# Optimization experiments

Hardware: AMD Instinct MI355X
Metric: run time of the kernel (lower is better)

Reference implementation:

```python
import jax, jax.numpy as jnp
import numpy as np

N = 100000
NFEAT = 128
NHID = 128
NCLASS = 40
E = 1600000
EPS = 1e-5


def _spmm(vals, src, dst, x, n):
    # y[dst] += vals * x[src]  (sparse adj @ x)
    return jax.ops.segment_sum(vals[:, None] * x[src], dst, num_segments=n)


def _bn(h, gamma, beta, rmean, rvar):
    # BatchNorm1d in eval mode (running statistics)
    return (h - rmean) * jax.lax.rsqrt(rvar + EPS) * gamma + beta


def setup_inputs() -> dict:
    key = jax.random.key(0)
    ks = jax.random.split(key, 24)
    inp = {
        'x': jax.random.normal(ks[0], (N, NFEAT), dtype=jnp.float32),
        'M': jax.random.uniform(ks[1], (N, 1), dtype=jnp.float32),
        'AM': jax.random.uniform(ks[2], (N, 1), dtype=jnp.float32),
        'srcZ': jax.random.randint(ks[3], (E,), 0, N, dtype=jnp.int32),
        'dstZ': jax.random.randint(ks[4], (E,), 0, N, dtype=jnp.int32),
        'valsZ': jax.random.uniform(ks[5], (E,), dtype=jnp.float32),
        'src': jax.random.randint(ks[6], (E,), 0, N, dtype=jnp.int32),
        'dst': jax.random.randint(ks[7], (E,), 0, N, dtype=jnp.int32),
        'vals': jax.random.uniform(ks[8], (E,), dtype=jnp.float32),
        # layer 0 (PaGConv) params
        'W0': jax.random.normal(ks[9], (NHID, NFEAT), dtype=jnp.float32) * (1.414 / np.sqrt(NFEAT)),
        'b0': jnp.zeros((NHID,), dtype=jnp.float32),
        'g0': jnp.ones((NHID,), dtype=jnp.float32),
        'be0': jnp.zeros((NHID,), dtype=jnp.float32),
        'rm0': jax.random.normal(ks[10], (NHID,), dtype=jnp.float32) * 0.1,
        'rv0': jax.random.uniform(ks[11], (NHID,), dtype=jnp.float32) + 0.5,
        # layer 1 (GConv) params
        'W1': jax.random.normal(ks[12], (NHID, NHID), dtype=jnp.float32) * (1.414 / np.sqrt(NHID)),
        'b1': jnp.zeros((NHID,), dtype=jnp.float32),
        'g1': jnp.ones((NHID,), dtype=jnp.float32),
        'be1': jnp.zeros((NHID,), dtype=jnp.float32),
        'rm1': jax.random.normal(ks[13], (NHID,), dtype=jnp.float32) * 0.1,
        'rv1': jax.random.uniform(ks[14], (NHID,), dtype=jnp.float32) + 0.5,
        # layer 2 (GConv) params
        'W2': jax.random.normal(ks[15], (NCLASS, NHID), dtype=jnp.float32) * (1.414 / np.sqrt(NHID)),
        'b2': jnp.zeros((NCLASS,), dtype=jnp.float32),
    }
    return inp


def reference(x, M, AM, srcZ, dstZ, valsZ, src, dst, vals,
              W0, b0, g0, be0, rm0, rv0,
              W1, b1, g1, be1, rm1, rv1,
              W2, b2):
    n = x.shape[0]
    # layer 0: PaGConv with adjZ: fc(spmm(adjZ, M*x) * AM), then BN + ReLU (dropout off in eval)
    h = _spmm(valsZ, srcZ, dstZ, M * x, n) * AM
    h = h @ W0.T + b0
    h = jax.nn.relu(_bn(h, g0, be0, rm0, rv0))
    # layer 1: GConv with adj: fc(spmm(adj, h)), then BN + ReLU
    h = _spmm(vals, src, dst, h, n)
    h = h @ W1.T + b1
    h = jax.nn.relu(_bn(h, g1, be1, rm1, rv1))
    # layer 2: GConv, then log_softmax
    h = _spmm(vals, src, dst, h, n)
    h = h @ W2.T + b2
    return jax.nn.log_softmax(h, axis=-1)
```

## Files before the change

kernel.cpp:

```cpp
#include <hip/hip_runtime.h>
#include <math.h>

#define NFEAT 128
#define NCLS 40
#define NCLSP 64
#define BINROWS 64
#define NBINMAX 1600
#define NBLKC 256
#define CHUNKMAX 6400
#define SEGC 7
#define RSMAX 2048

typedef short bf16x8 __attribute__((ext_vector_type(8)));
typedef float f32x4 __attribute__((ext_vector_type(4)));

__device__ __forceinline__ float bf2f(unsigned int lo16) {
  return __uint_as_float((lo16 & 0xffffu) << 16);
}
__device__ __forceinline__ unsigned int f2bf(float x) {
  unsigned int u = __float_as_uint(x);
  return (u + 0x7fffu + ((u >> 16) & 1u)) >> 16;
}

__global__ __launch_bounds__(256) void prep_all(
    const float* b0, const float* g0, const float* be0,
    const float* rm0, const float* rv0,
    const float* b1, const float* g1, const float* be1,
    const float* rm1, const float* rv1,
    float* sc0, float* sh0, float* sc1, float* sh1,
    const float* __restrict__ W0, const float* __restrict__ W1,
    const float* __restrict__ W2,
    unsigned short* __restrict__ Wb0, unsigned short* __restrict__ Wb1,
    unsigned short* __restrict__ W2hi, unsigned short* __restrict__ W2lo,
    const float* __restrict__ x, const float* __restrict__ Mv,
    unsigned short* __restrict__ xm, int n) {
  int t = threadIdx.x;
  if (blockIdx.x == 0) {
    if (t < 128) {
      float s = g0[t] * rsqrtf(rv0[t] + 1e-5f);
      sc0[t] = s;
      sh0[t] = (b0[t] - rm0[t]) * s + be0[t];
    } else {
      int i = t - 128;
      float s = g1[i] * rsqrtf(rv1[i] + 1e-5f);
      sc1[i] = s;
      sh1[i] = (b1[i] - rm1[i]) * s + be1[i];
    }
    return;
  }
  if (blockIdx.x <= 20) {
    int i = (blockIdx.x - 1) * 256 + t;
    if (i < 4096) {
      const float* W = (i < 2048) ? W0 : W1;
      unsigned short* Wb = (i < 2048) ? Wb0 : Wb1;
      int j = (i < 2048) ? i : i - 2048;
      const float4* p = (const float4*)(W + (size_t)j * 8);
      float4 v0 = p[0], v1 = p[1];
      unsigned int o0 = f2bf(v0.x) | (f2bf(v0.y) << 16);
      unsigned int o1 = f2bf(v0.z) | (f2bf(v0.w) << 16);
      unsigned int o2 = f2bf(v1.x) | (f2bf(v1.y) << 16);
      unsigned int o3 = f2bf(v1.z) | (f2bf(v1.w) << 16);
      ((uint4*)Wb)[j] = make_uint4(o0, o1, o2, o3);
    } else {
      int j = i - 4096;
      int r = j >> 4;
      float v[8] = {0.f, 0.f, 0.f, 0.f, 0.f, 0.f, 0.f, 0.f};
      if (r < NCLS) {
        const float4* p = (const float4*)(W2 + (size_t)j * 8);
        float4 a = p[0], b = p[1];
        v[0] = a.x; v[1] = a.y; v[2] = a.z; v[3] = a.w;
        v[4] = b.x; v[5] = b.y; v[6] = b.z; v[7] = b.w;
      }
      unsigned int h[8], l[8];
#pragma unroll
      for (int q = 0; q < 8; ++q) {
        h[q] = f2bf(v[q]);
        l[q] = f2bf(v[q] - bf2f(h[q]));
      }
      ((uint4*)W2hi)[j] = make_uint4(h[0] | (h[1] << 16), h[2] | (h[3] << 16),
                                     h[4] | (h[5] << 16), h[6] | (h[7] << 16));
      ((uint4*)W2lo)[j] = make_uint4(l[0] | (l[1] << 16), l[2] | (l[3] << 16),
                                     l[4] | (l[5] << 16), l[6] | (l[7] << 16));
    }
    return;
  }
  int i = (blockIdx.x - 21) * 256 + t;
  if (i >= n * (NFEAT / 8)) return;
  int row = i >> 4;
  float m = Mv[row];
  const float4* p = (const float4*)(x + (size_t)i * 8);
  float4 v0 = p[0], v1 = p[1];
  unsigned int o0 = f2bf(v0.x * m) | (f2bf(v0.y * m) << 16);
  unsigned int o1 = f2bf(v0.z * m) | (f2bf(v0.w * m) << 16);
  unsigned int o2 = f2bf(v1.x * m) | (f2bf(v1.y * m) << 16);
  unsigned int o3 = f2bf(v1.z * m) | (f2bf(v1.w * m) << 16);
  ((uint4*)xm)[i] = make_uint4(o0, o1, o2, o3);
}

__global__ __launch_bounds__(256) void bin_sort2(
    const int* __restrict__ srcZ, const int* __restrict__ dstZ, const float* __restrict__ valZ,
    const int* __restrict__ srcA, const int* __restrict__ dstA, const float* __restrict__ valA,
    int2* __restrict__ DrmZ, int2* __restrict__ DrmA,
    int2* __restrict__ binsCZ, int2* __restrict__ binsCA,
    int E, int nbin, int chunk) {
  __shared__ int2 stage[CHUNKMAX];
  __shared__ int cur[NBINMAX];
  __shared__ int ps[256];
  const int t = threadIdx.x;
  int k = blockIdx.x;
  const int* srcp; const int* dstp; const float* valp; int2* Drm; int2* binsC;
  if (k < NBLKC) {
    srcp = srcZ; dstp = dstZ; valp = valZ; Drm = DrmZ; binsC = binsCZ;
  } else {
    k -= NBLKC;
    srcp = srcA; dstp = dstA; valp = valA; Drm = DrmA; binsC = binsCA;
  }
  for (int i = t; i < nbin; i += 256) cur[i] = 0;
  __syncthreads();
  const int e0 = k * chunk, e1 = min(E, e0 + chunk);
#pragma unroll 4
  for (int e = e0 + t; e < e1; e += 256) atomicAdd(&cur[dstp[e] >> 6], 1);
  __syncthreads();
  int loc[SEGC], cnt[SEGC];
  int s = 0;
#pragma unroll
  for (int j = 0; j < SEGC; ++j) {
    int i = t * SEGC + j;
    int v = (i < nbin) ? cur[i] : 0;
    loc[j] = s; cnt[j] = v;
    s += v;
  }
  ps[t] = s;
  __syncthreads();
  for (int o = 1; o < 256; o <<= 1) {
    int x = (t >= o) ? ps[t - o] : 0;
    __syncthreads();
    ps[t] += x;
    __syncthreads();
  }
  int ex = ps[t] - s;
#pragma unroll
  for (int j = 0; j < SEGC; ++j) {
    int i = t * SEGC + j;
    if (i < nbin) {
      int o = ex + loc[j];
      Drm[(size_t)k * nbin + i] = make_int2(e0 + o, cnt[j]);
      cur[i] = o;
    }
  }
  __syncthreads();
#pragma unroll 2
  for (int e = e0 + t; e < e1; e += 256) {
    int d = dstp[e];
    int p = atomicAdd(&cur[d >> 6], 1);
    stage[p] = make_int2(srcp[e] | ((d & 63) << 17), __float_as_int(valp[e]));
  }
  __syncthreads();
  const int n = e1 - e0;
  for (int i = t; i < n; i += 256) binsC[e0 + i] = stage[i];
}

__global__ __launch_bounds__(256) void row_sort2(
    const int2* __restrict__ DrmZ, const int2* __restrict__ DrmA,
    const int2* __restrict__ binsCZ, const int2* __restrict__ binsCA,
    int2* __restrict__ bins2Z, int2* __restrict__ bins2A,
    int2* __restrict__ rdZ, int2* __restrict__ rdA, int n, int nbin) {
  __shared__ int2 stage[RSMAX];
  __shared__ int ps[256];
  __shared__ int rcnt[BINROWS];
  __shared__ int roff[BINROWS];
  int b = blockIdx.x;
  const int t = threadIdx.x;
  const int2* Drm; const int2* binsC; int2* bins2; int2* rowdesc;
  if (b < nbin) {
    Drm = DrmZ; binsC = binsCZ; bins2 = bins2Z; rowdesc = rdZ;
  } else {
    b -= nbin;
    Drm = DrmA; binsC = binsCA; bins2 = bins2A; rowdesc = rdA;
  }
  if (t < BINROWS) rcnt[t] = 0;
  int2 run = Drm[(size_t)t * nbin + b];
  ps[t] = run.y;
  __syncthreads();
  for (int o = 1; o < 256; o <<= 1) {
    int x = (t >= o) ? ps[t - o] : 0;
    __syncthreads();
    ps[t] += x;
    __syncthreads();
  }
  int mystart = ps[t] - run.y;
  for (int j = 0; j < run.y; ++j) {
    int2 en = binsC[run.x + j];
    int idx = mystart + j;
    if (idx < RSMAX) stage[idx] = en;
    atomicAdd(&rcnt[(en.x >> 17) & 63], 1);
  }
  __syncthreads();
  const int bs = b * RSMAX;
  if (t < BINROWS) {
    int c = rcnt[t];
    int s = c;
#pragma unroll
    for (int o = 1; o < 64; o <<= 1) {
      int v = __shfl_up(s, o);
      if (t >= o) s += v;
    }
    int excl = s - c;
    int row = b * BINROWS + t;
    if (row < n) rowdesc[row] = make_int2(bs + excl, c);
    roff[t] = excl;
  }
  __syncthreads();
  int total = min(ps[255], RSMAX);
  for (int i = t; i < total; i += 256) {
    int2 en = stage[i];
    int row = (en.x >> 17) & 63;
    int p = atomicAdd(&roff[row], 1);
    bins2[bs + p] = en;
  }
}

template <bool SCALE>
__global__ __launch_bounds__(256) void spmm128_sorted(
    const int2* __restrict__ rowdesc, const int2* __restrict__ bins2,
    const unsigned short* __restrict__ X, const float* __restrict__ AM,
    unsigned short* __restrict__ Y, int n) {
  int row = (blockIdx.x * 256 + threadIdx.x) >> 6;
  int lane = threadIdx.x & 63;
  if (row >= n) return;
  int2 rd = rowdesc[row];
  int s = rd.x, d = rd.y;
  int half = lane >> 5, l32 = lane & 31;
  float s0 = 0.f, s1 = 0.f, s2 = 0.f, s3 = 0.f;
  for (int kb = 0; kb < d; kb += 64) {
    int rem = min(64, d - kb);
    int2 my = (lane < rem) ? bins2[s + kb + lane] : make_int2(0, 0);
    int myc = my.x & 0x1FFFF;
    float myw = __int_as_float(my.y);
    for (int k = 0; k < rem; k += 8) {
#pragma unroll
      for (int st = 0; st < 4; ++st) {
        int idx = k + 2 * st + half;
        int c = __shfl(myc, idx);
        float wv = __shfl(myw, idx);
        uint2 pv = *(const uint2*)(X + (size_t)c * NFEAT + l32 * 4);
        s0 += wv * bf2f(pv.x);
        s1 += wv * bf2f(pv.x >> 16);
        s2 += wv * bf2f(pv.y);
        s3 += wv * bf2f(pv.y >> 16);
      }
    }
  }
  s0 += __shfl_xor(s0, 32); s1 += __shfl_xor(s1, 32);
  s2 += __shfl_xor(s2, 32); s3 += __shfl_xor(s3, 32);
  if (SCALE) {
    float am = AM[row];
    s0 *= am; s1 *= am; s2 *= am; s3 *= am;
  }
  unsigned int pk = half ? (f2bf(s2) | (f2bf(s3) << 16)) : (f2bf(s0) | (f2bf(s1) << 16));
  ((unsigned int*)Y)[(size_t)row * (NFEAT / 2) + l32 * 2 + half] = pk;
}

template <bool FUSE_G2>
__global__ __launch_bounds__(256) void gemm_mfma128(
    const unsigned short* __restrict__ Y, const unsigned short* __restrict__ Wb,
    const float* __restrict__ scale, const float* __restrict__ shift,
    unsigned short* __restrict__ Out,
    const unsigned short* __restrict__ Whi, const unsigned short* __restrict__ Wlo,
    unsigned short* __restrict__ G2, int M) {
  const int wave = threadIdx.x >> 6;
  const int lane = threadIdx.x & 63;
  const int quad = lane >> 4;
  const int l16 = lane & 15;
  const int arow = blockIdx.x * 64 + wave * 16 + l16;
  const bool rv = arow < M;

  f32x4 acc[8];
#pragma unroll
  for (int c = 0; c < 8; ++c) acc[c] = (f32x4){0.f, 0.f, 0.f, 0.f};

#pragma unroll
  for (int kc = 0; kc < 128; kc += 32) {
    bf16x8 a = rv ? *(const bf16x8*)(Y + (size_t)arow * 128 + kc + quad * 8)
                  : (bf16x8){0, 0, 0, 0, 0, 0, 0, 0};
#pragma unroll
    for (int c = 0; c < 8; ++c) {
      bf16x8 b = *(const bf16x8*)(Wb + (size_t)(c * 16 + l16) * 128 + kc + quad * 8);
      acc[c] = __builtin_amdgcn_mfma_f32_16x16x32_bf16(a, b, acc[c], 0, 0, 0);
    }
  }

  const int orow0 = blockIdx.x * 64 + wave * 16 + quad * 4;

  if constexpr (!FUSE_G2) {
#pragma unroll
    for (int c = 0; c < 8; ++c) {
      int col = c * 16 + l16;
      float sc = scale[col], sh = shift[col];
#pragma unroll
      for (int r = 0; r < 4; ++r) {
        int orow = orow0 + r;
        if (orow < M) {
          float v = fmaxf(acc[c][r] * sc + sh, 0.f);
          Out[(size_t)orow * 128 + col] = (unsigned short)f2bf(v);
        }
      }
    }
  } else {
    __shared__ unsigned short Ht[64][136];
    const int lrow0 = wave * 16 + quad * 4;
#pragma unroll
    for (int c = 0; c < 8; ++c) {
      int col = c * 16 + l16;
      float sc = scale[col], sh = shift[col];
#pragma unroll
      for (int r = 0; r < 4; ++r) {
        float v = fmaxf(acc[c][r] * sc + sh, 0.f);
        Ht[lrow0 + r][col] = (unsigned short)f2bf(v);
      }
    }
    __syncthreads();
    bf16x8 af[4];
#pragma unroll
    for (int kc = 0; kc < 4; ++kc)
      af[kc] = *(const bf16x8*)(&Ht[wave * 16 + l16][kc * 32 + quad * 8]);
    f32x4 acc2[4];
#pragma unroll
    for (int c2 = 0; c2 < 4; ++c2) acc2[c2] = (f32x4){0.f, 0.f, 0.f, 0.f};
#pragma unroll
    for (int kc = 0; kc < 4; ++kc) {
#pragma unroll
      for (int c2 = 0; c2 < 4; ++c2) {
        bf16x8 bh = *(const bf16x8*)(Whi + (size_t)(c2 * 16 + l16) * 128 + kc * 32 + quad * 8);
        bf16x8 bl = *(const bf16x8*)(Wlo + (size_t)(c2 * 16 + l16) * 128 + kc * 32 + quad * 8);
        acc2[c2] = __builtin_amdgcn_mfma_f32_16x16x32_bf16(af[kc], bh, acc2[c2], 0, 0, 0);
        acc2[c2] = __builtin_amdgcn_mfma_f32_16x16x32_bf16(af[kc], bl, acc2[c2], 0, 0, 0);
      }
    }
#pragma unroll
    for (int c2 = 0; c2 < 4; ++c2) {
      int col = c2 * 16 + l16;
#pragma unroll
      for (int r = 0; r < 4; ++r) {
        int orow = orow0 + r;
        if (orow < M) G2[(size_t)orow * NCLSP + col] = (unsigned short)f2bf(acc2[c2][r]);
      }
    }
  }
}

__global__ __launch_bounds__(256) void spmm_softmax64(
    const int2* __restrict__ rowdesc, const int2* __restrict__ bins2,
    const unsigned short* __restrict__ G2, const float* __restrict__ b2,
    float* __restrict__ out, int n) {
  int row = (blockIdx.x * 256 + threadIdx.x) >> 6;
  int lane = threadIdx.x & 63;
  if (row >= n) return;
  const int eidx = lane >> 4, q = lane & 15;
  const bool vq = q < (NCLS / 4);
  float4 bv = vq ? *(const float4*)(b2 + q * 4) : make_float4(0.f, 0.f, 0.f, 0.f);

  int2 rdv = rowdesc[row];
  int s0i = rdv.x, d = rdv.y;
  float a0 = 0.f, a1 = 0.f, a2 = 0.f, a3 = 0.f;
  for (int kb = 0; kb < d; kb += 64) {
    int rem = min(64, d - kb);
    int2 my = (lane < rem) ? bins2[s0i + kb + lane] : make_int2(0, 0);
    int myc = my.x & 0x1FFFF;
    float myw = __int_as_float(my.y);
    int steps = (rem + 3) >> 2;
#pragma unroll 4
    for (int st = 0; st < steps; ++st) {
      int idx = st * 4 + eidx;
      int c = __shfl(myc, idx);
      float wv = __shfl(myw, idx);
      uint2 pv = *(const uint2*)(G2 + (size_t)c * NCLSP + q * 4);
      a0 += wv * bf2f(pv.x);
      a1 += wv * bf2f(pv.x >> 16);
      a2 += wv * bf2f(pv.y);
      a3 += wv * bf2f(pv.y >> 16);
    }
  }
  a0 += __shfl_xor(a0, 16); a1 += __shfl_xor(a1, 16);
  a2 += __shfl_xor(a2, 16); a3 += __shfl_xor(a3, 16);
  a0 += __shfl_xor(a0, 32); a1 += __shfl_xor(a1, 32);
  a2 += __shfl_xor(a2, 32); a3 += __shfl_xor(a3, 32);
  float z0 = a0 + bv.x, z1 = a1 + bv.y, z2 = a2 + bv.z, z3 = a3 + bv.w;
  bool par = (eidx == 0) && vq;
  float m = par ? fmaxf(fmaxf(z0, z1), fmaxf(z2, z3)) : -INFINITY;
#pragma unroll
  for (int o = 1; o < 64; o <<= 1) m = fmaxf(m, __shfl_xor(m, o));
  float ex = par ? (__expf(z0 - m) + __expf(z1 - m) + __expf(z2 - m) + __expf(z3 - m)) : 0.f;
#pragma unroll
  for (int o = 1; o < 64; o <<= 1) ex += __shfl_xor(ex, o);
  float lg = m + __logf(ex);
  if (par) {
    *(float4*)&out[(size_t)row * NCLS + q * 4] =
        make_float4(z0 - lg, z1 - lg, z2 - lg, z3 - lg);
  }
}


extern "C" void kernel_launch(void* const* d_in, const int* in_sizes, int n_in,
                              void* d_out, int out_size, void* d_ws, size_t ws_size,
                              hipStream_t stream) {
  const float* x    = (const float*)d_in[0];
  const float* Mv   = (const float*)d_in[1];
  const float* AM   = (const float*)d_in[2];
  const int* srcZ   = (const int*)d_in[3];
  const int* dstZ   = (const int*)d_in[4];
  const float* valsZ= (const float*)d_in[5];
  const int* src    = (const int*)d_in[6];
  const int* dst    = (const int*)d_in[7];
  const float* vals = (const float*)d_in[8];
  const float* W0   = (const float*)d_in[9];
  const float* b0   = (const float*)d_in[10];
  const float* g0   = (const float*)d_in[11];
  const float* be0  = (const float*)d_in[12];
  const float* rm0  = (const float*)d_in[13];
  const float* rv0  = (const float*)d_in[14];
  const float* W1   = (const float*)d_in[15];
  const float* b1   = (const float*)d_in[16];
  const float* g1   = (const float*)d_in[17];
  const float* be1  = (const float*)d_in[18];
  const float* rm1  = (const float*)d_in[19];
  const float* rv1  = (const float*)d_in[20];
  const float* W2   = (const float*)d_in[21];
  const float* b2   = (const float*)d_in[22];
  float* out = (float*)d_out;

  const int N = in_sizes[1];
  const int E = in_sizes[3];
  const int NBIN = (N + BINROWS - 1) / BINROWS;
  const int CHUNK = (E + NBLKC - 1) / NBLKC;

  char* w = (char*)d_ws;
  size_t off = 0;
  auto alloc = [&](size_t bytes) -> void* {
    void* p = w + off;
    off = (off + bytes + 255) & ~(size_t)255;
    return p;
  };
  const size_t bins2Bytes = (size_t)NBIN * RSMAX * 8;
  const size_t bufBytes = (size_t)N * NFEAT * 2;
  int2* binsCZ = (int2*)alloc((size_t)NBLKC * CHUNK * 8);
  int2* binsCA = (int2*)alloc((size_t)NBLKC * CHUNK * 8);
  int2* bins2A = (int2*)alloc(bins2Bytes);
  int2* rdZ = (int2*)alloc((size_t)N * 8);
  int2* rdA = (int2*)alloc((size_t)N * 8);
  unsigned short* xm = (unsigned short*)alloc(bufBytes);
  unsigned short* bufA = (unsigned short*)alloc(bufBytes);
  unsigned short* bufB = (unsigned short*)alloc(bins2Bytes > bufBytes ? bins2Bytes : bufBytes);
  float* sc0 = (float*)alloc(128 * 4);
  float* sh0 = (float*)alloc(128 * 4);
  float* sc1 = (float*)alloc(128 * 4);
  float* sh1 = (float*)alloc(128 * 4);
  unsigned short* Wb0 = (unsigned short*)alloc(128 * 128 * 2);
  unsigned short* Wb1 = (unsigned short*)alloc(128 * 128 * 2);
  unsigned short* W2hi = (unsigned short*)alloc(64 * 128 * 2);
  unsigned short* W2lo = (unsigned short*)alloc(64 * 128 * 2);
  const size_t drmBytes = (size_t)NBLKC * NBIN * 8;
  int2* DrmZ = (int2*)((char*)bufA + 0 * drmBytes);
  int2* DrmA = (int2*)((char*)bufA + 1 * drmBytes);
  int2* bins2Z = (int2*)bufB;
  unsigned short* G2 = bufB;

  const int RB = (N + 3) / 4;
  const int GB64 = (N + 63) / 64;
  const int CONVB = (N * (NFEAT / 8) + 255) / 256;

  prep_all<<<21 + CONVB, 256, 0, stream>>>(b0, g0, be0, rm0, rv0, b1, g1, be1, rm1, rv1,
                                           sc0, sh0, sc1, sh1, W0, W1, W2,
                                           Wb0, Wb1, W2hi, W2lo, x, Mv, xm, N);

  bin_sort2<<<2 * NBLKC, 256, 0, stream>>>(srcZ, dstZ, valsZ, src, dst, vals,
                                           DrmZ, DrmA, binsCZ, binsCA, E, NBIN, CHUNK);
  row_sort2<<<2 * NBIN, 256, 0, stream>>>(DrmZ, DrmA, binsCZ, binsCA,
                                          bins2Z, bins2A, rdZ, rdA, N, NBIN);

  spmm128_sorted<true><<<RB, 256, 0, stream>>>(rdZ, bins2Z, xm, AM, bufA, N);
  gemm_mfma128<false><<<GB64, 256, 0, stream>>>(bufA, Wb0, sc0, sh0, bufB,
                                                nullptr, nullptr, nullptr, N);

  spmm128_sorted<false><<<RB, 256, 0, stream>>>(rdA, bins2A, bufB,
                                                (const float*)nullptr, bufA, N);
  gemm_mfma128<true><<<GB64, 256, 0, stream>>>(bufA, Wb1, sc1, sh1, nullptr,
                                               W2hi, W2lo, G2, N);

  spmm_softmax64<<<RB, 256, 0, stream>>>(rdA, bins2A, G2, b2, out, N);
}
```

Measured before the change: 507.0 us.

## Cache atomic ranks in bin/row sorts and shrink SpMM blocks to 128 threads

In bin_sort2, each edge's bin, in-row index and atomic rank are packed into registers during the counting pass. The scatter pass then computes its position from the scanned offset plus that rank, so it no longer re-reads dst or runs a second round of shared atomics. row_sort2 likewise records each entry's rank from the counting atomic into a shared short array and scatters without a second atomicAdd. Separately, the SpMM and softmax kernels drop to 128-thread blocks (two rows per block) for finer scheduling granularity. The changes cost more registers (25 packed ints per thread) and extra shared memory, and the packed layout assumes at most 8191 edges per bin per chunk.

Measured after the change: 505.1 us. No clear change (-0.4%).

```diff
diff --git a/kernel.cpp b/kernel.cpp
--- a/kernel.cpp
+++ b/kernel.cpp
@@ -8,6 +8,7 @@
 #define NBINMAX 1600
 #define NBLKC 256
 #define CHUNKMAX 6400
+#define CEDGE 25
 #define SEGC 7
 #define RSMAX 2048
 
@@ -118,8 +119,17 @@
   for (int i = t; i < nbin; i += 256) cur[i] = 0;
   __syncthreads();
   const int e0 = k * chunk, e1 = min(E, e0 + chunk);
-#pragma unroll 4
-  for (int e = e0 + t; e < e1; e += 256) atomicAdd(&cur[dstp[e] >> 6], 1);
+  int pk[CEDGE];
+#pragma unroll
+  for (int j = 0; j < CEDGE; ++j) {
+    int e = e0 + t + j * 256;
+    if (e < e1) {
+      int d = dstp[e];
+      int bin = d >> 6;
+      int r = atomicAdd(&cur[bin], 1);
+      pk[j] = (bin << 19) | ((d & 63) << 13) | r;
+    }
+  }
   __syncthreads();
   int loc[SEGC], cnt[SEGC];
   int s = 0;
@@ -149,11 +159,14 @@
     }
   }
   __syncthreads();
-#pragma unroll 2
-  for (int e = e0 + t; e < e1; e += 256) {
-    int d = dstp[e];
-    int p = atomicAdd(&cur[d >> 6], 1);
-    stage[p] = make_int2(srcp[e] | ((d & 63) << 17), __float_as_int(valp[e]));
+#pragma unroll
+  for (int j = 0; j < CEDGE; ++j) {
+    int e = e0 + t + j * 256;
+    if (e < e1) {
+      int v = pk[j];
+      int p = cur[(unsigned)v >> 19] + (v & 0x1FFF);
+      stage[p] = make_int2(srcp[e] | (((v >> 13) & 63) << 17), __float_as_int(valp[e]));
+    }
   }
   __syncthreads();
   const int n = e1 - e0;
@@ -166,6 +179,7 @@
     int2* __restrict__ bins2Z, int2* __restrict__ bins2A,
     int2* __restrict__ rdZ, int2* __restrict__ rdA, int n, int nbin) {
   __shared__ int2 stage[RSMAX];
+  __shared__ short rankArr[RSMAX];
   __shared__ int ps[256];
   __shared__ int rcnt[BINROWS];
   __shared__ int roff[BINROWS];
@@ -192,8 +206,11 @@
   for (int j = 0; j < run.y; ++j) {
     int2 en = binsC[run.x + j];
     int idx = mystart + j;
-    if (idx < RSMAX) stage[idx] = en;
-    atomicAdd(&rcnt[(en.x >> 17) & 63], 1);
+    int r = atomicAdd(&rcnt[(en.x >> 17) & 63], 1);
+    if (idx < RSMAX) {
+      stage[idx] = en;
+      rankArr[idx] = (short)r;
+    }
   }
   __syncthreads();
   const int bs = b * RSMAX;
@@ -215,17 +232,16 @@
   for (int i = t; i < total; i += 256) {
     int2 en = stage[i];
     int row = (en.x >> 17) & 63;
-    int p = atomicAdd(&roff[row], 1);
-    bins2[bs + p] = en;
+    bins2[bs + roff[row] + rankArr[i]] = en;
   }
 }
 
 template <bool SCALE>
-__global__ __launch_bounds__(256) void spmm128_sorted(
+__global__ __launch_bounds__(128) void spmm128_sorted(
     const int2* __restrict__ rowdesc, const int2* __restrict__ bins2,
     const unsigned short* __restrict__ X, const float* __restrict__ AM,
     unsigned short* __restrict__ Y, int n) {
-  int row = (blockIdx.x * 256 + threadIdx.x) >> 6;
+  int row = (blockIdx.x * 128 + threadIdx.x) >> 6;
   int lane = threadIdx.x & 63;
   if (row >= n) return;
   int2 rd = rowdesc[row];
@@ -349,11 +365,11 @@
   }
 }
 
-__global__ __launch_bounds__(256) void spmm_softmax64(
+__global__ __launch_bounds__(128) void spmm_softmax64(
     const int2* __restrict__ rowdesc, const int2* __restrict__ bins2,
     const unsigned short* __restrict__ G2, const float* __restrict__ b2,
     float* __restrict__ out, int n) {
-  int row = (blockIdx.x * 256 + threadIdx.x) >> 6;
+  int row = (blockIdx.x * 128 + threadIdx.x) >> 6;
   int lane = threadIdx.x & 63;
   if (row >= n) return;
   const int eidx = lane >> 4, q = lane & 15;
@@ -465,7 +481,7 @@
   int2* bins2Z = (int2*)bufB;
   unsigned short* G2 = bufB;
 
-  const int RB = (N + 3) / 4;
+  const int RB2 = (N + 1) / 2;
   const int GB64 = (N + 63) / 64;
   const int CONVB = (N * (NFEAT / 8) + 255) / 256;
 
@@ -478,14 +494,14 @@
   row_sort2<<<2 * NBIN, 256, 0, stream>>>(DrmZ, DrmA, binsCZ, binsCA,
                                           bins2Z, bins2A, rdZ, rdA, N, NBIN);
 
-  spmm128_sorted<true><<<RB, 256, 0, stream>>>(rdZ, bins2Z, xm, AM, bufA, N);
+  spmm128_sorted<true><<<RB2, 128, 0, stream>>>(rdZ, bins2Z, xm, AM, bufA, N);
   gemm_mfma128<false><<<GB64, 256, 0, stream>>>(bufA, Wb0, sc0, sh0, bufB,
                                                 nullptr, nullptr, nullptr, N);
 
-  spmm128_sorted<false><<<RB, 256, 0, stream>>>(rdA, bins2A, bufB,
-                                                (const float*)nullptr, bufA, N);
+  spmm128_sorted<false><<<RB2, 128, 0, stream>>>(rdA, bins2A, bufB,
+                                                 (const float*)nullptr, bufA, N);
   gemm_mfma128<true><<<GB64, 256, 0, stream>>>(bufA, Wb1, sc1, sh1, nullptr,
                                                W2hi, W2lo, G2, N);
 
-  spmm_softmax64<<<RB, 256, 0, stream>>>(rdA, bins2A, G2, b2, out, N);
-}
+  spmm_softmax64<<<RB2, 128, 0, stream>>>(rdA, bins2A, G2, b2, out, N);
+}
```
